# Performance work log

Hardware: AMD Instinct MI355X
Metric: run time of the kernel (lower is better)

The kernel has to match this reference:

```python
import jax, jax.numpy as jnp
import numpy as np

N = 50000
E = 800000
IN_DIM = 128
HIDDEN = 256
HEADS = 8
HEAD_DIM = HIDDEN // HEADS  # 32
NUM_CLASSES = 40
NEG_SLOPE = 0.2


def setup_inputs() -> dict:
    key = jax.random.key(0)
    ks = jax.random.split(key, 16)
    x = jax.random.normal(ks[0], (N, IN_DIM), dtype=jnp.float32)
    edge_index = jax.random.randint(ks[1], (2, E), 0, N, dtype=jnp.int64)

    def glorot(k, shape, fan_in):
        return jax.random.normal(k, shape, dtype=jnp.float32) / np.sqrt(fan_in)

    # layer 1: in -> heads*head_dim (concat)
    W1 = glorot(ks[2], (IN_DIM, HEADS * HEAD_DIM), IN_DIM)
    as1 = glorot(ks[3], (HEADS, HEAD_DIM), HEAD_DIM)
    ad1 = glorot(ks[4], (HEADS, HEAD_DIM), HEAD_DIM)
    b1 = jnp.zeros((HEADS * HEAD_DIM,), dtype=jnp.float32)
    # layer 2: hidden -> heads*head_dim (concat)
    W2 = glorot(ks[5], (HIDDEN, HEADS * HEAD_DIM), HIDDEN)
    as2 = glorot(ks[6], (HEADS, HEAD_DIM), HEAD_DIM)
    ad2 = glorot(ks[7], (HEADS, HEAD_DIM), HEAD_DIM)
    b2 = jnp.zeros((HEADS * HEAD_DIM,), dtype=jnp.float32)
    # layer 3: hidden -> num_classes, 1 head, no concat (mean == identity for 1 head)
    W3 = glorot(ks[8], (HIDDEN, 1 * NUM_CLASSES), HIDDEN)
    as3 = glorot(ks[9], (1, NUM_CLASSES), NUM_CLASSES)
    ad3 = glorot(ks[10], (1, NUM_CLASSES), NUM_CLASSES)
    b3 = jnp.zeros((NUM_CLASSES,), dtype=jnp.float32)
    return {"x": x, "edge_index": edge_index,
            "W1": W1, "as1": as1, "ad1": ad1, "b1": b1,
            "W2": W2, "as2": as2, "ad2": ad2, "b2": b2,
            "W3": W3, "as3": as3, "ad3": ad3, "b3": b3}


def _segment_softmax(logits, seg, n):
    # logits: [E, H]; softmax per destination node
    m = jax.ops.segment_max(logits, seg, num_segments=n)
    m = jnp.where(jnp.isfinite(m), m, 0.0)  # empty segments -> 0
    e = jnp.exp(logits - m[seg])
    s = jax.ops.segment_sum(e, seg, num_segments=n)
    return e / (s[seg] + 1e-16)


def _gat_layer(x, src, dst, W, a_src, a_dst, b, heads, concat):
    n = x.shape[0]
    h = (x @ W).reshape(n, heads, -1)                    # [N, H, D]
    al_s = jnp.einsum('nhd,hd->nh', h, a_src)            # [N, H]
    al_d = jnp.einsum('nhd,hd->nh', h, a_dst)            # [N, H]
    e = jax.nn.leaky_relu(al_s[src] + al_d[dst], NEG_SLOPE)  # [E, H]
    alpha = _segment_softmax(e, dst, n)                  # [E, H]
    msg = h[src] * alpha[..., None]                      # [E, H, D]
    out = jax.ops.segment_sum(msg, dst, num_segments=n)  # [N, H, D]
    out = out.reshape(n, -1) if concat else out.mean(axis=1)
    return out + b


def reference(x, edge_index, W1, as1, ad1, b1, W2, as2, ad2, b2, W3, as3, ad3, b3):
    # add self loops (PyG GATConv default)
    loops = jnp.arange(N, dtype=edge_index.dtype)
    src = jnp.concatenate([edge_index[0], loops])
    dst = jnp.concatenate([edge_index[1], loops])
    # eval mode: dropout is a no-op
    h = _gat_layer(x, src, dst, W1, as1, ad1, b1, HEADS, True)
    h = jax.nn.elu(h)
    h = _gat_layer(h, src, dst, W2, as2, ad2, b2, HEADS, True)
    h = jax.nn.elu(h)
    out = _gat_layer(h, src, dst, W3, as3, ad3, b3, 1, False)
    return out
```

## Files before the change

### kernel.cpp

```cpp
#include <hip/hip_runtime.h>
#include <hip/hip_bf16.h>

#define NEG_SLOPE 0.2f

typedef __attribute__((ext_vector_type(8))) short bf16x8;
typedef __attribute__((ext_vector_type(4))) float f32x4;

__device__ __forceinline__ unsigned short f2bf(float v) {
    union { float f; unsigned int u; } x; x.f = v;
    unsigned int r = x.u + 0x7fffu + ((x.u >> 16) & 1u);
    return (unsigned short)(r >> 16);
}
__device__ __forceinline__ float bf2f(unsigned short b) {
    union { unsigned int u; float f; } x; x.u = ((unsigned int)b) << 16;
    return x.f;
}


__global__ void count_edges_k(const int* __restrict__ ei, int E, int n, int* __restrict__ cnt) {
    int e = blockIdx.x * 256 + threadIdx.x;
    int ET = E + n;
    if (e >= ET) return;
    int d = (e < E) ? ei[E + e] : (e - E);
    atomicAdd(&cnt[d], 1);
}

__global__ void scan1_k(const int* __restrict__ cnt, int* __restrict__ row_ptr,
                        int* __restrict__ bsums, int n) {
    __shared__ int sd[256];
    int b = blockIdx.x, t = threadIdx.x;
    int base = b * 1024 + t * 4;
    int v[4];
    int loc = 0;
#pragma unroll
    for (int j = 0; j < 4; ++j) {
        v[j] = (base + j < n) ? cnt[base + j] : 0;
        loc += v[j];
    }
    sd[t] = loc;
    __syncthreads();
    for (int off = 1; off < 256; off <<= 1) {
        int x = (t >= off) ? sd[t - off] : 0;
        __syncthreads();
        sd[t] += x;
        __syncthreads();
    }
    int run = sd[t] - loc;
    if (t == 255) bsums[b] = sd[t];
#pragma unroll
    for (int j = 0; j < 4; ++j) {
        if (base + j < n) row_ptr[base + j] = run;
        run += v[j];
    }
}

__global__ void scan2_k(int* __restrict__ bsums, int nb) {
    if (threadIdx.x == 0 && blockIdx.x == 0) {
        int run = 0;
        for (int i = 0; i < nb; ++i) { int x = bsums[i]; bsums[i] = run; run += x; }
    }
}

__global__ void scan3_k(int* __restrict__ row_ptr, int* __restrict__ pos,
                        const int* __restrict__ bsums, int n, int total) {
    int idx = blockIdx.x * 256 + threadIdx.x;
    if (idx < n) {
        int vv = row_ptr[idx] + bsums[idx >> 10];
        row_ptr[idx] = vv;
        pos[idx] = vv;
    } else if (idx == n) {
        row_ptr[n] = total;
    }
}

__global__ void scatter_edges_k(const int* __restrict__ ei, int E, int n,
                                int* __restrict__ pos, int* __restrict__ srcs) {
    int e = blockIdx.x * 256 + threadIdx.x;
    int ET = E + n;
    if (e >= ET) return;
    int s, d;
    if (e < E) { s = ei[e]; d = ei[E + e]; }
    else       { s = e - E; d = e - E; }
    int idx = atomicAdd(&pos[d], 1);
    srcs[idx] = s;
}


#define R1 (128 * 256)
#define R2 (256 * 256)
#define R3 (256 * 128)

__global__ void convert_w_all_k(const float* __restrict__ W1, const float* __restrict__ W2,
                                const float* __restrict__ W3,
                                unsigned short* __restrict__ b1h, unsigned short* __restrict__ b1l,
                                unsigned short* __restrict__ b2h, unsigned short* __restrict__ b2l,
                                unsigned short* __restrict__ b3h, unsigned short* __restrict__ b3l) {
    int idx = blockIdx.x * 256 + threadIdx.x;
    float v;
    unsigned short* dh;
    unsigned short* dl;
    int o;
    if (idx < R1) {
        int k = idx >> 8, c = idx & 255;
        v = W1[idx]; dh = b1h; dl = b1l; o = c * 128 + k;
    } else if (idx < R1 + R2) {
        int j = idx - R1;
        int k = j >> 8, c = j & 255;
        v = W2[j]; dh = b2h; dl = b2l; o = c * 256 + k;
    } else if (idx < R1 + R2 + R3) {
        int j = idx - (R1 + R2);
        int k = j >> 7, c = j & 127;
        v = (c < 40) ? W3[k * 40 + c] : 0.f;
        dh = b3h; dl = b3l; o = c * 256 + k;
    } else {
        return;
    }
    unsigned short h = f2bf(v);
    dh[o] = h;
    dl[o] = f2bf(v - bf2f(h));
}


#define GPAD 40

__global__ __launch_bounds__(256) void mfma_gemm_k(const float* __restrict__ A,
                                                   const unsigned short* __restrict__ Bh,
                                                   const unsigned short* __restrict__ Bl,
                                                   unsigned short* __restrict__ Cb,
                                                   int M, int K, int Nc) {
    __shared__ unsigned short Ash[128][GPAD];
    __shared__ unsigned short Asl[128][GPAD];
    __shared__ unsigned short Bsh[128][GPAD];
    __shared__ unsigned short Bsl[128][GPAD];

    int bm = blockIdx.y * 128;
    int bn = blockIdx.x * 128;
    int t = threadIdx.x;
    int w = t >> 6, l = t & 63;
    int wm = w >> 1, wn = w & 1;
    int lr = l & 15, lk = (l >> 4) * 8;

    int srow = t >> 1;
    int skh  = (t & 1) * 16;

    f32x4 acc[4][4];
#pragma unroll
    for (int i = 0; i < 4; ++i)
#pragma unroll
        for (int j = 0; j < 4; ++j)
            acc[i][j] = (f32x4){0.f, 0.f, 0.f, 0.f};

    const int arow = bm + srow;
    const bool arow_ok = (arow < M);
    const size_t acol_base = (size_t)arow * K + skh;
    const size_t bcol_base = (size_t)(bn + srow) * K + skh;

    for (int k0 = 0; k0 < K; k0 += 32) {
        float vv[16];
        if (arow_ok) {
            const float4* ap = reinterpret_cast<const float4*>(A + acol_base + k0);
#pragma unroll
            for (int q = 0; q < 4; ++q) {
                float4 v4 = ap[q];
                vv[4 * q + 0] = v4.x; vv[4 * q + 1] = v4.y;
                vv[4 * q + 2] = v4.z; vv[4 * q + 3] = v4.w;
            }
        } else {
#pragma unroll
            for (int q = 0; q < 16; ++q) vv[q] = 0.f;
        }
        unsigned int hw[8], lw[8];
#pragma unroll
        for (int q = 0; q < 8; ++q) {
            unsigned short h0 = f2bf(vv[2 * q]);
            unsigned short h1 = f2bf(vv[2 * q + 1]);
            unsigned short l0 = f2bf(vv[2 * q] - bf2f(h0));
            unsigned short l1 = f2bf(vv[2 * q + 1] - bf2f(h1));
            hw[q] = (unsigned int)h0 | ((unsigned int)h1 << 16);
            lw[q] = (unsigned int)l0 | ((unsigned int)l1 << 16);
        }
        __syncthreads();
        {
            uint4* dh = reinterpret_cast<uint4*>(&Ash[srow][skh]);
            uint4* dl = reinterpret_cast<uint4*>(&Asl[srow][skh]);
            dh[0] = make_uint4(hw[0], hw[1], hw[2], hw[3]);
            dh[1] = make_uint4(hw[4], hw[5], hw[6], hw[7]);
            dl[0] = make_uint4(lw[0], lw[1], lw[2], lw[3]);
            dl[1] = make_uint4(lw[4], lw[5], lw[6], lw[7]);
        }
        {
            const uint4* sh = reinterpret_cast<const uint4*>(Bh + bcol_base + k0);
            const uint4* sl = reinterpret_cast<const uint4*>(Bl + bcol_base + k0);
            uint4* dh = reinterpret_cast<uint4*>(&Bsh[srow][skh]);
            uint4* dl = reinterpret_cast<uint4*>(&Bsl[srow][skh]);
            dh[0] = sh[0]; dh[1] = sh[1];
            dl[0] = sl[0]; dl[1] = sl[1];
        }
        __syncthreads();

        bf16x8 ah[4], al[4], bh[4], bl[4];
#pragma unroll
        for (int i = 0; i < 4; ++i) {
            int r = wm * 64 + i * 16 + lr;
            ah[i] = *reinterpret_cast<const bf16x8*>(&Ash[r][lk]);
            al[i] = *reinterpret_cast<const bf16x8*>(&Asl[r][lk]);
        }
#pragma unroll
        for (int j = 0; j < 4; ++j) {
            int c = wn * 64 + j * 16 + lr;
            bh[j] = *reinterpret_cast<const bf16x8*>(&Bsh[c][lk]);
            bl[j] = *reinterpret_cast<const bf16x8*>(&Bsl[c][lk]);
        }
#pragma unroll
        for (int i = 0; i < 4; ++i)
#pragma unroll
            for (int j = 0; j < 4; ++j) {
                acc[i][j] = __builtin_amdgcn_mfma_f32_16x16x32_bf16(ah[i], bh[j], acc[i][j], 0, 0, 0);
                acc[i][j] = __builtin_amdgcn_mfma_f32_16x16x32_bf16(ah[i], bl[j], acc[i][j], 0, 0, 0);
                acc[i][j] = __builtin_amdgcn_mfma_f32_16x16x32_bf16(al[i], bh[j], acc[i][j], 0, 0, 0);
            }
    }

#pragma unroll
    for (int i = 0; i < 4; ++i) {
#pragma unroll
        for (int r = 0; r < 4; ++r) {
            int row_g = bm + wm * 64 + i * 16 + (l >> 4) * 4 + r;
            if (row_g >= M) continue;
#pragma unroll
            for (int j = 0; j < 4; ++j) {
                int col_g = bn + wn * 64 + j * 16 + lr;
                Cb[(size_t)row_g * Nc + col_g] = f2bf(acc[i][j][r]);
            }
        }
    }
}


__global__ __launch_bounds__(256) void gemm_bf16a_k(const unsigned short* __restrict__ A,
                                                    const unsigned short* __restrict__ Bh,
                                                    const unsigned short* __restrict__ Bl,
                                                    unsigned short* __restrict__ Cb,
                                                    int M, int K, int Nc) {
    __shared__ unsigned short As[128][GPAD];
    __shared__ unsigned short Bsh[128][GPAD];
    __shared__ unsigned short Bsl[128][GPAD];

    int bm = blockIdx.y * 128;
    int bn = blockIdx.x * 128;
    int t = threadIdx.x;
    int w = t >> 6, l = t & 63;
    int wm = w >> 1, wn = w & 1;
    int lr = l & 15, lk = (l >> 4) * 8;

    int srow = t >> 1;
    int skh  = (t & 1) * 16;

    f32x4 acc[4][4];
#pragma unroll
    for (int i = 0; i < 4; ++i)
#pragma unroll
        for (int j = 0; j < 4; ++j)
            acc[i][j] = (f32x4){0.f, 0.f, 0.f, 0.f};

    const int arow = bm + srow;
    const bool arow_ok = (arow < M);
    const size_t acol_base = (size_t)arow * K + skh;
    const size_t bcol_base = (size_t)(bn + srow) * K + skh;

    for (int k0 = 0; k0 < K; k0 += 32) {
        __syncthreads();
        {
            uint4* da = reinterpret_cast<uint4*>(&As[srow][skh]);
            if (arow_ok) {
                const uint4* sa = reinterpret_cast<const uint4*>(A + acol_base + k0);
                da[0] = sa[0]; da[1] = sa[1];
            } else {
                da[0] = make_uint4(0u, 0u, 0u, 0u);
                da[1] = make_uint4(0u, 0u, 0u, 0u);
            }
            const uint4* sh = reinterpret_cast<const uint4*>(Bh + bcol_base + k0);
            const uint4* sl = reinterpret_cast<const uint4*>(Bl + bcol_base + k0);
            uint4* dh = reinterpret_cast<uint4*>(&Bsh[srow][skh]);
            uint4* dl = reinterpret_cast<uint4*>(&Bsl[srow][skh]);
            dh[0] = sh[0]; dh[1] = sh[1];
            dl[0] = sl[0]; dl[1] = sl[1];
        }
        __syncthreads();

        bf16x8 ah[4], bh[4], bl[4];
#pragma unroll
        for (int i = 0; i < 4; ++i) {
            int r = wm * 64 + i * 16 + lr;
            ah[i] = *reinterpret_cast<const bf16x8*>(&As[r][lk]);
        }
#pragma unroll
        for (int j = 0; j < 4; ++j) {
            int c = wn * 64 + j * 16 + lr;
            bh[j] = *reinterpret_cast<const bf16x8*>(&Bsh[c][lk]);
            bl[j] = *reinterpret_cast<const bf16x8*>(&Bsl[c][lk]);
        }
#pragma unroll
        for (int i = 0; i < 4; ++i)
#pragma unroll
            for (int j = 0; j < 4; ++j) {
                acc[i][j] = __builtin_amdgcn_mfma_f32_16x16x32_bf16(ah[i], bh[j], acc[i][j], 0, 0, 0);
                acc[i][j] = __builtin_amdgcn_mfma_f32_16x16x32_bf16(ah[i], bl[j], acc[i][j], 0, 0, 0);
            }
    }

#pragma unroll
    for (int i = 0; i < 4; ++i) {
#pragma unroll
        for (int r = 0; r < 4; ++r) {
            int row_g = bm + wm * 64 + i * 16 + (l >> 4) * 4 + r;
            if (row_g >= M) continue;
#pragma unroll
            for (int j = 0; j < 4; ++j) {
                int col_g = bn + wn * 64 + j * 16 + lr;
                Cb[(size_t)row_g * Nc + col_g] = f2bf(acc[i][j][r]);
            }
        }
    }
}


__global__ __launch_bounds__(256) void compute_al_k(const unsigned short* __restrict__ h,
                                                    const float* __restrict__ a_src,
                                                    const float* __restrict__ a_dst,
                                                    float* __restrict__ al_s,
                                                    float* __restrict__ al_d, int n) {
    int gw = blockIdx.x * 4 + (threadIdx.x >> 6);
    int nw = gridDim.x * 4;
    int lane = threadIdx.x & 63;
    float4 asv = reinterpret_cast<const float4*>(a_src)[lane];
    float4 adv = reinterpret_cast<const float4*>(a_dst)[lane];
    for (int node = gw; node < n; node += nw) {
        ushort4 v = reinterpret_cast<const ushort4*>(h + (size_t)node * 256)[lane];
        float ps = bf2f(v.x) * asv.x + bf2f(v.y) * asv.y + bf2f(v.z) * asv.z + bf2f(v.w) * asv.w;
        float pd = bf2f(v.x) * adv.x + bf2f(v.y) * adv.y + bf2f(v.z) * adv.z + bf2f(v.w) * adv.w;
#pragma unroll
        for (int off = 1; off < 8; off <<= 1) {
            ps += __shfl_xor(ps, off, 64);
            pd += __shfl_xor(pd, off, 64);
        }
        if ((lane & 7) == 0) {
            al_s[node * 8 + (lane >> 3)] = ps;
            al_d[node * 8 + (lane >> 3)] = pd;
        }
    }
}

__global__ void compute_al3_k(const unsigned short* __restrict__ h,
                              const float* __restrict__ a_src, const float* __restrict__ a_dst,
                              float* __restrict__ al_s, float* __restrict__ al_d, int n) {
    int wid = threadIdx.x >> 6, lane = threadIdx.x & 63;
    int node = blockIdx.x * 4 + wid;
    if (node >= n) return;
    float hv = (lane < 40) ? bf2f(h[(size_t)node * 128 + lane]) : 0.f;
    float ps = (lane < 40) ? hv * a_src[lane] : 0.f;
    float pd = (lane < 40) ? hv * a_dst[lane] : 0.f;
#pragma unroll
    for (int off = 32; off; off >>= 1) {
        ps += __shfl_xor(ps, off, 64);
        pd += __shfl_xor(pd, off, 64);
    }
    if (lane == 0) { al_s[node] = ps; al_d[node] = pd; }
}


__global__ __launch_bounds__(256) void edge_softmax_k(const float* __restrict__ al_s,
                                                      const float* __restrict__ al_d,
                                                      const int* __restrict__ row_ptr,
                                                      const int* __restrict__ srcs,
                                                      float* __restrict__ w,
                                                      float* __restrict__ inv, int n8) {
    int tid = blockIdx.x * 256 + threadIdx.x;
    if (tid >= n8) return;
    int dst = tid >> 3, hd = tid & 7;
    int beg = row_ptr[dst], end = row_ptr[dst + 1];
    float ald = al_d[tid];

    float m = -1e30f;
    int i = beg;
    for (; i + 2 <= end; i += 2) {
        int s0 = srcs[i], s1 = srcs[i + 1];
        float l0 = al_s[s0 * 8 + hd] + ald;
        float l1 = al_s[s1 * 8 + hd] + ald;
        l0 = (l0 > 0.f) ? l0 : NEG_SLOPE * l0;
        l1 = (l1 > 0.f) ? l1 : NEG_SLOPE * l1;
        m = fmaxf(m, fmaxf(l0, l1));
    }
    if (i < end) {
        int s0 = srcs[i];
        float l0 = al_s[s0 * 8 + hd] + ald;
        l0 = (l0 > 0.f) ? l0 : NEG_SLOPE * l0;
        m = fmaxf(m, l0);
    }

    float sw = 0.f;
    i = beg;
    for (; i + 2 <= end; i += 2) {
        int s0 = srcs[i], s1 = srcs[i + 1];
        float l0 = al_s[s0 * 8 + hd] + ald;
        float l1 = al_s[s1 * 8 + hd] + ald;
        l0 = (l0 > 0.f) ? l0 : NEG_SLOPE * l0;
        l1 = (l1 > 0.f) ? l1 : NEG_SLOPE * l1;
        float e0 = __expf(l0 - m);
        float e1 = __expf(l1 - m);
        w[(size_t)i * 8 + hd] = e0;
        w[(size_t)(i + 1) * 8 + hd] = e1;
        sw += e0 + e1;
    }
    if (i < end) {
        int s = srcs[i];
        float l = al_s[s * 8 + hd] + ald;
        l = (l > 0.f) ? l : NEG_SLOPE * l;
        float e = __expf(l - m);
        w[(size_t)i * 8 + hd] = e;
        sw += e;
    }
    inv[tid] = 1.f / (sw + 1e-16f);
}

__global__ __launch_bounds__(256) void edge_softmax3_k(const float* __restrict__ al_s,
                                                       const float* __restrict__ al_d,
                                                       const int* __restrict__ row_ptr,
                                                       const int* __restrict__ srcs,
                                                       float* __restrict__ w,
                                                       float* __restrict__ inv, int n) {
    int dst = blockIdx.x * 256 + threadIdx.x;
    if (dst >= n) return;
    int beg = row_ptr[dst], end = row_ptr[dst + 1];
    float ald = al_d[dst];

    float m = -1e30f;
    int i = beg;
    for (; i + 2 <= end; i += 2) {
        int s0 = srcs[i], s1 = srcs[i + 1];
        float l0 = al_s[s0] + ald;
        float l1 = al_s[s1] + ald;
        l0 = (l0 > 0.f) ? l0 : NEG_SLOPE * l0;
        l1 = (l1 > 0.f) ? l1 : NEG_SLOPE * l1;
        m = fmaxf(m, fmaxf(l0, l1));
    }
    if (i < end) {
        int s0 = srcs[i];
        float l0 = al_s[s0] + ald;
        l0 = (l0 > 0.f) ? l0 : NEG_SLOPE * l0;
        m = fmaxf(m, l0);
    }

    float sw = 0.f;
    for (i = beg; i < end; ++i) {
        int s = srcs[i];
        float l = al_s[s] + ald;
        l = (l > 0.f) ? l : NEG_SLOPE * l;
        float e = __expf(l - m);
        w[i] = e;
        sw += e;
    }
    inv[dst] = 1.f / (sw + 1e-16f);
}


template <bool ELU>
__global__ __launch_bounds__(256) void gat_gather_k(const unsigned short* __restrict__ h,
                                                    const float* __restrict__ w,
                                                    const float* __restrict__ inv,
                                                    const int* __restrict__ row_ptr,
                                                    const int* __restrict__ srcs,
                                                    const float* __restrict__ bias,
                                                    unsigned short* __restrict__ out, int n) {
    int gw = blockIdx.x * 4 + (threadIdx.x >> 6);
    int nw = gridDim.x * 4;
    int lane = threadIdx.x & 63;
    int hd = lane >> 3;
    const ushort4* hp = reinterpret_cast<const ushort4*>(h);
    float4 b4 = reinterpret_cast<const float4*>(bias)[lane];

    for (int dst = gw; dst < n; dst += nw) {
        int beg = row_ptr[dst], end = row_ptr[dst + 1];
        float4 acc = make_float4(0.f, 0.f, 0.f, 0.f);
        int i = beg;
        for (; i + 4 <= end; i += 4) {
            int s0 = srcs[i + 0], s1 = srcs[i + 1], s2 = srcs[i + 2], s3 = srcs[i + 3];
            float w0 = w[(size_t)(i + 0) * 8 + hd];
            float w1 = w[(size_t)(i + 1) * 8 + hd];
            float w2 = w[(size_t)(i + 2) * 8 + hd];
            float w3 = w[(size_t)(i + 3) * 8 + hd];
            ushort4 v0 = hp[(size_t)s0 * 64 + lane];
            ushort4 v1 = hp[(size_t)s1 * 64 + lane];
            ushort4 v2 = hp[(size_t)s2 * 64 + lane];
            ushort4 v3 = hp[(size_t)s3 * 64 + lane];
            acc.x = fmaf(w0, bf2f(v0.x), acc.x);
            acc.y = fmaf(w0, bf2f(v0.y), acc.y);
            acc.z = fmaf(w0, bf2f(v0.z), acc.z);
            acc.w = fmaf(w0, bf2f(v0.w), acc.w);
            acc.x = fmaf(w1, bf2f(v1.x), acc.x);
            acc.y = fmaf(w1, bf2f(v1.y), acc.y);
            acc.z = fmaf(w1, bf2f(v1.z), acc.z);
            acc.w = fmaf(w1, bf2f(v1.w), acc.w);
            acc.x = fmaf(w2, bf2f(v2.x), acc.x);
            acc.y = fmaf(w2, bf2f(v2.y), acc.y);
            acc.z = fmaf(w2, bf2f(v2.z), acc.z);
            acc.w = fmaf(w2, bf2f(v2.w), acc.w);
            acc.x = fmaf(w3, bf2f(v3.x), acc.x);
            acc.y = fmaf(w3, bf2f(v3.y), acc.y);
            acc.z = fmaf(w3, bf2f(v3.z), acc.z);
            acc.w = fmaf(w3, bf2f(v3.w), acc.w);
        }
        for (; i < end; ++i) {
            int s = srcs[i];
            float wgt = w[(size_t)i * 8 + hd];
            ushort4 v = hp[(size_t)s * 64 + lane];
            acc.x = fmaf(wgt, bf2f(v.x), acc.x);
            acc.y = fmaf(wgt, bf2f(v.y), acc.y);
            acc.z = fmaf(wgt, bf2f(v.z), acc.z);
            acc.w = fmaf(wgt, bf2f(v.w), acc.w);
        }

        float iv = inv[dst * 8 + hd];
        float4 o;
        o.x = acc.x * iv + b4.x;
        o.y = acc.y * iv + b4.y;
        o.z = acc.z * iv + b4.z;
        o.w = acc.w * iv + b4.w;
        if (ELU) {
            o.x = (o.x > 0.f) ? o.x : expm1f(o.x);
            o.y = (o.y > 0.f) ? o.y : expm1f(o.y);
            o.z = (o.z > 0.f) ? o.z : expm1f(o.z);
            o.w = (o.w > 0.f) ? o.w : expm1f(o.w);
        }
        ushort4 ob;
        ob.x = f2bf(o.x); ob.y = f2bf(o.y); ob.z = f2bf(o.z); ob.w = f2bf(o.w);
        reinterpret_cast<ushort4*>(out + (size_t)dst * 256)[lane] = ob;
    }
}

__global__ __launch_bounds__(256) void gat_gather3_k(const unsigned short* __restrict__ h,
                                                     const float* __restrict__ w,
                                                     const float* __restrict__ inv,
                                                     const int* __restrict__ row_ptr,
                                                     const int* __restrict__ srcs,
                                                     const float* __restrict__ bias,
                                                     float* __restrict__ out, int n) {
    int gw = blockIdx.x * 4 + (threadIdx.x >> 6);
    int nw = gridDim.x * 4;
    int lane = threadIdx.x & 63;
    int es = lane >> 4, cl = lane & 15;

    for (int dst = gw; dst < n; dst += nw) {
        int beg = row_ptr[dst], end = row_ptr[dst + 1];
        float4 acc = make_float4(0.f, 0.f, 0.f, 0.f);
        for (int i = beg; i < end; i += 4) {
            int idx = i + es;
            bool ok = (idx < end);
            int s = ok ? srcs[idx] : srcs[beg];
            float wgt = ok ? w[idx] : 0.f;
            ushort4 v = reinterpret_cast<const ushort4*>(h + (size_t)s * 128)[cl];
            acc.x = fmaf(wgt, bf2f(v.x), acc.x);
            acc.y = fmaf(wgt, bf2f(v.y), acc.y);
            acc.z = fmaf(wgt, bf2f(v.z), acc.z);
            acc.w = fmaf(wgt, bf2f(v.w), acc.w);
        }
#pragma unroll
        for (int off = 16; off <= 32; off <<= 1) {
            acc.x += __shfl_xor(acc.x, off, 64);
            acc.y += __shfl_xor(acc.y, off, 64);
            acc.z += __shfl_xor(acc.z, off, 64);
            acc.w += __shfl_xor(acc.w, off, 64);
        }
        if (es == 0 && cl < 10) {
            float iv = inv[dst];
            int c = cl * 4;
            float4 b4 = *reinterpret_cast<const float4*>(bias + c);
            float4 o;
            o.x = acc.x * iv + b4.x;
            o.y = acc.y * iv + b4.y;
            o.z = acc.z * iv + b4.z;
            o.w = acc.w * iv + b4.w;
            *reinterpret_cast<float4*>(out + (size_t)dst * 40 + c) = o;
        }
    }
}


extern "C" void kernel_launch(void* const* d_in, const int* in_sizes, int n_in,
                              void* d_out, int out_size, void* d_ws, size_t ws_size,
                              hipStream_t stream) {
    const float* x   = (const float*)d_in[0];
    const int*   ei  = (const int*)d_in[1];
    const float* W1  = (const float*)d_in[2];
    const float* as1 = (const float*)d_in[3];
    const float* ad1 = (const float*)d_in[4];
    const float* b1  = (const float*)d_in[5];
    const float* W2  = (const float*)d_in[6];
    const float* as2 = (const float*)d_in[7];
    const float* ad2 = (const float*)d_in[8];
    const float* b2  = (const float*)d_in[9];
    const float* W3  = (const float*)d_in[10];
    const float* as3 = (const float*)d_in[11];
    const float* ad3 = (const float*)d_in[12];
    const float* b3  = (const float*)d_in[13];

    const int N = in_sizes[0] / 128;
    const int E = in_sizes[1] / 2;
    const int ET = E + N;

    char* ws = (char*)d_ws;
    size_t off = 0;
    auto alloc = [&](size_t bytes) -> void* {
        void* p = ws + off;
        off += (bytes + 255) & ~(size_t)255;
        return p;
    };
    int*   row_ptr = (int*)alloc(sizeof(int) * (N + 1));
    int*   pos     = (int*)alloc(sizeof(int) * N);
    int*   srcs    = (int*)alloc(sizeof(int) * ET);
    int*   bsums   = (int*)alloc(sizeof(int) * 64);
    float* als     = (float*)alloc(sizeof(float) * N * 8);
    float* ald     = (float*)alloc(sizeof(float) * N * 8);
    float* wbuf    = (float*)alloc(sizeof(float) * (size_t)ET * 8);
    float* invb    = (float*)alloc(sizeof(float) * N * 8);
    unsigned short* hb16 = (unsigned short*)alloc(sizeof(unsigned short) * (size_t)N * 256);
    unsigned short* ab16 = (unsigned short*)alloc(sizeof(unsigned short) * (size_t)N * 256);
    unsigned short* wb1h = (unsigned short*)alloc(sizeof(unsigned short) * 128 * 256);
    unsigned short* wb1l = (unsigned short*)alloc(sizeof(unsigned short) * 128 * 256);
    unsigned short* wb2h = (unsigned short*)alloc(sizeof(unsigned short) * 256 * 256);
    unsigned short* wb2l = (unsigned short*)alloc(sizeof(unsigned short) * 256 * 256);
    unsigned short* wb3h = (unsigned short*)alloc(sizeof(unsigned short) * 128 * 256);
    unsigned short* wb3l = (unsigned short*)alloc(sizeof(unsigned short) * 128 * 256);
    (void)ws_size;

    const int nb = (N + 1023) / 1024;
    const int PG = 2048;

    convert_w_all_k<<<(R1 + R2 + R3 + 255) / 256, 256, 0, stream>>>(
        W1, W2, W3, wb1h, wb1l, wb2h, wb2l, wb3h, wb3l);

    hipMemsetAsync(pos, 0, sizeof(int) * N, stream);
    count_edges_k<<<(ET + 255) / 256, 256, 0, stream>>>(ei, E, N, pos);
    scan1_k<<<nb, 256, 0, stream>>>(pos, row_ptr, bsums, N);
    scan2_k<<<1, 64, 0, stream>>>(bsums, nb);
    scan3_k<<<(N + 1 + 255) / 256, 256, 0, stream>>>(row_ptr, pos, bsums, N, ET);
    scatter_edges_k<<<(ET + 255) / 256, 256, 0, stream>>>(ei, E, N, pos, srcs);

    const int gy = (N + 127) / 128;
    const int gagg = (N + 3) / 4;
    const int gsm = (N * 8 + 255) / 256;

    mfma_gemm_k<<<dim3(2, gy), 256, 0, stream>>>(x, wb1h, wb1l, hb16, N, 128, 256);
    compute_al_k<<<PG, 256, 0, stream>>>(hb16, as1, ad1, als, ald, N);
    edge_softmax_k<<<gsm, 256, 0, stream>>>(als, ald, row_ptr, srcs, wbuf, invb, N * 8);
    gat_gather_k<true><<<PG, 256, 0, stream>>>(hb16, wbuf, invb, row_ptr, srcs, b1, ab16, N);

    gemm_bf16a_k<<<dim3(2, gy), 256, 0, stream>>>(ab16, wb2h, wb2l, hb16, N, 256, 256);
    compute_al_k<<<PG, 256, 0, stream>>>(hb16, as2, ad2, als, ald, N);
    edge_softmax_k<<<gsm, 256, 0, stream>>>(als, ald, row_ptr, srcs, wbuf, invb, N * 8);
    gat_gather_k<true><<<PG, 256, 0, stream>>>(hb16, wbuf, invb, row_ptr, srcs, b2, ab16, N);

    gemm_bf16a_k<<<dim3(1, gy), 256, 0, stream>>>(ab16, wb3h, wb3l, hb16, N, 256, 128);
    compute_al3_k<<<gagg, 256, 0, stream>>>(hb16, as3, ad3, als, ald, N);
    edge_softmax3_k<<<(N + 255) / 256, 256, 0, stream>>>(als, ald, row_ptr, srcs, wbuf, invb, N);
    gat_gather3_k<<<PG, 256, 0, stream>>>(hb16, wbuf, invb, row_ptr, srcs, b3, (float*)d_out, N);
}
```

Measured before the change: 427.6 us.

## Parallelize edge softmax per wave and process destination pairs in gather

Edge softmax moves from one thread per (node, head) to one wavefront per node, with lanes strided over edges and shuffle reductions for max and sum. This is meant to fix load imbalance and uncoalesced serial loops over high-degree nodes. The layer-1/2 gather now handles two destination nodes per wave with interleaved predicated 4-edge batches, raising memory-level parallelism. The pair kernel assumes N is even and wastes loads when the two degrees differ; empty segments would read endA-1 out of range, but self-loops rule that out.

Measured after the change: 440.9 us. 1.03x slower.

```diff
diff --git a/kernel.cpp b/kernel.cpp
--- a/kernel.cpp
+++ b/kernel.cpp
@@ -369,109 +369,90 @@
 }
 
 
-__global__ __launch_bounds__(256) void edge_softmax_k(const float* __restrict__ al_s,
-                                                      const float* __restrict__ al_d,
-                                                      const int* __restrict__ row_ptr,
-                                                      const int* __restrict__ srcs,
-                                                      float* __restrict__ w,
-                                                      float* __restrict__ inv, int n8) {
-    int tid = blockIdx.x * 256 + threadIdx.x;
-    if (tid >= n8) return;
-    int dst = tid >> 3, hd = tid & 7;
-    int beg = row_ptr[dst], end = row_ptr[dst + 1];
-    float ald = al_d[tid];
-
-    float m = -1e30f;
-    int i = beg;
-    for (; i + 2 <= end; i += 2) {
-        int s0 = srcs[i], s1 = srcs[i + 1];
-        float l0 = al_s[s0 * 8 + hd] + ald;
-        float l1 = al_s[s1 * 8 + hd] + ald;
-        l0 = (l0 > 0.f) ? l0 : NEG_SLOPE * l0;
-        l1 = (l1 > 0.f) ? l1 : NEG_SLOPE * l1;
-        m = fmaxf(m, fmaxf(l0, l1));
-    }
-    if (i < end) {
-        int s0 = srcs[i];
-        float l0 = al_s[s0 * 8 + hd] + ald;
-        l0 = (l0 > 0.f) ? l0 : NEG_SLOPE * l0;
-        m = fmaxf(m, l0);
-    }
-
-    float sw = 0.f;
-    i = beg;
-    for (; i + 2 <= end; i += 2) {
-        int s0 = srcs[i], s1 = srcs[i + 1];
-        float l0 = al_s[s0 * 8 + hd] + ald;
-        float l1 = al_s[s1 * 8 + hd] + ald;
-        l0 = (l0 > 0.f) ? l0 : NEG_SLOPE * l0;
-        l1 = (l1 > 0.f) ? l1 : NEG_SLOPE * l1;
-        float e0 = __expf(l0 - m);
-        float e1 = __expf(l1 - m);
-        w[(size_t)i * 8 + hd] = e0;
-        w[(size_t)(i + 1) * 8 + hd] = e1;
-        sw += e0 + e1;
-    }
-    if (i < end) {
-        int s = srcs[i];
-        float l = al_s[s * 8 + hd] + ald;
-        l = (l > 0.f) ? l : NEG_SLOPE * l;
-        float e = __expf(l - m);
-        w[(size_t)i * 8 + hd] = e;
-        sw += e;
-    }
-    inv[tid] = 1.f / (sw + 1e-16f);
-}
-
-__global__ __launch_bounds__(256) void edge_softmax3_k(const float* __restrict__ al_s,
-                                                       const float* __restrict__ al_d,
-                                                       const int* __restrict__ row_ptr,
-                                                       const int* __restrict__ srcs,
-                                                       float* __restrict__ w,
-                                                       float* __restrict__ inv, int n) {
-    int dst = blockIdx.x * 256 + threadIdx.x;
-    if (dst >= n) return;
-    int beg = row_ptr[dst], end = row_ptr[dst + 1];
-    float ald = al_d[dst];
-
-    float m = -1e30f;
-    int i = beg;
-    for (; i + 2 <= end; i += 2) {
-        int s0 = srcs[i], s1 = srcs[i + 1];
-        float l0 = al_s[s0] + ald;
-        float l1 = al_s[s1] + ald;
-        l0 = (l0 > 0.f) ? l0 : NEG_SLOPE * l0;
-        l1 = (l1 > 0.f) ? l1 : NEG_SLOPE * l1;
-        m = fmaxf(m, fmaxf(l0, l1));
-    }
-    if (i < end) {
-        int s0 = srcs[i];
-        float l0 = al_s[s0] + ald;
-        l0 = (l0 > 0.f) ? l0 : NEG_SLOPE * l0;
-        m = fmaxf(m, l0);
-    }
-
-    float sw = 0.f;
-    for (i = beg; i < end; ++i) {
-        int s = srcs[i];
-        float l = al_s[s] + ald;
-        l = (l > 0.f) ? l : NEG_SLOPE * l;
-        float e = __expf(l - m);
-        w[i] = e;
-        sw += e;
-    }
-    inv[dst] = 1.f / (sw + 1e-16f);
+__global__ __launch_bounds__(256) void edge_softmax_wave_k(const float* __restrict__ al_s,
+                                                           const float* __restrict__ al_d,
+                                                           const int* __restrict__ row_ptr,
+                                                           const int* __restrict__ srcs,
+                                                           float* __restrict__ w,
+                                                           float* __restrict__ inv, int n) {
+    int gw = blockIdx.x * 4 + (threadIdx.x >> 6);
+    int nw = gridDim.x * 4;
+    int lane = threadIdx.x & 63;
+    int es = lane >> 3, hd = lane & 7;
+    for (int dst = gw; dst < n; dst += nw) {
+        int beg = row_ptr[dst], end = row_ptr[dst + 1];
+        float ald = al_d[dst * 8 + hd];
+        float m = -1e30f;
+        for (int i = beg + es; i < end; i += 8) {
+            int s = srcs[i];
+            float l = al_s[s * 8 + hd] + ald;
+            l = (l > 0.f) ? l : NEG_SLOPE * l;
+            m = fmaxf(m, l);
+        }
+        m = fmaxf(m, __shfl_xor(m, 8, 64));
+        m = fmaxf(m, __shfl_xor(m, 16, 64));
+        m = fmaxf(m, __shfl_xor(m, 32, 64));
+        float sw = 0.f;
+        for (int i = beg + es; i < end; i += 8) {
+            int s = srcs[i];
+            float l = al_s[s * 8 + hd] + ald;
+            l = (l > 0.f) ? l : NEG_SLOPE * l;
+            float e = __expf(l - m);
+            w[(size_t)i * 8 + hd] = e;
+            sw += e;
+        }
+        sw += __shfl_xor(sw, 8, 64);
+        sw += __shfl_xor(sw, 16, 64);
+        sw += __shfl_xor(sw, 32, 64);
+        if (es == 0) inv[dst * 8 + hd] = 1.f / (sw + 1e-16f);
+    }
+}
+
+__global__ __launch_bounds__(256) void edge_softmax3_wave_k(const float* __restrict__ al_s,
+                                                            const float* __restrict__ al_d,
+                                                            const int* __restrict__ row_ptr,
+                                                            const int* __restrict__ srcs,
+                                                            float* __restrict__ w,
+                                                            float* __restrict__ inv, int n) {
+    int gw = blockIdx.x * 4 + (threadIdx.x >> 6);
+    int nw = gridDim.x * 4;
+    int lane = threadIdx.x & 63;
+    for (int dst = gw; dst < n; dst += nw) {
+        int beg = row_ptr[dst], end = row_ptr[dst + 1];
+        float ald = al_d[dst];
+        float m = -1e30f;
+        for (int i = beg + lane; i < end; i += 64) {
+            int s = srcs[i];
+            float l = al_s[s] + ald;
+            l = (l > 0.f) ? l : NEG_SLOPE * l;
+            m = fmaxf(m, l);
+        }
+#pragma unroll
+        for (int off = 32; off; off >>= 1) m = fmaxf(m, __shfl_xor(m, off, 64));
+        float sw = 0.f;
+        for (int i = beg + lane; i < end; i += 64) {
+            int s = srcs[i];
+            float l = al_s[s] + ald;
+            l = (l > 0.f) ? l : NEG_SLOPE * l;
+            float e = __expf(l - m);
+            w[i] = e;
+            sw += e;
+        }
+#pragma unroll
+        for (int off = 32; off; off >>= 1) sw += __shfl_xor(sw, off, 64);
+        if (lane == 0) inv[dst] = 1.f / (sw + 1e-16f);
+    }
 }
 
 
 template <bool ELU>
-__global__ __launch_bounds__(256) void gat_gather_k(const unsigned short* __restrict__ h,
-                                                    const float* __restrict__ w,
-                                                    const float* __restrict__ inv,
-                                                    const int* __restrict__ row_ptr,
-                                                    const int* __restrict__ srcs,
-                                                    const float* __restrict__ bias,
-                                                    unsigned short* __restrict__ out, int n) {
+__global__ __launch_bounds__(256) void gat_gather_pair_k(const unsigned short* __restrict__ h,
+                                                         const float* __restrict__ w,
+                                                         const float* __restrict__ inv,
+                                                         const int* __restrict__ row_ptr,
+                                                         const int* __restrict__ srcs,
+                                                         const float* __restrict__ bias,
+                                                         unsigned short* __restrict__ out, int npairs) {
     int gw = blockIdx.x * 4 + (threadIdx.x >> 6);
     int nw = gridDim.x * 4;
     int lane = threadIdx.x & 63;
@@ -479,62 +460,73 @@
     const ushort4* hp = reinterpret_cast<const ushort4*>(h);
     float4 b4 = reinterpret_cast<const float4*>(bias)[lane];
 
-    for (int dst = gw; dst < n; dst += nw) {
-        int beg = row_ptr[dst], end = row_ptr[dst + 1];
-        float4 acc = make_float4(0.f, 0.f, 0.f, 0.f);
-        int i = beg;
-        for (; i + 4 <= end; i += 4) {
-            int s0 = srcs[i + 0], s1 = srcs[i + 1], s2 = srcs[i + 2], s3 = srcs[i + 3];
-            float w0 = w[(size_t)(i + 0) * 8 + hd];
-            float w1 = w[(size_t)(i + 1) * 8 + hd];
-            float w2 = w[(size_t)(i + 2) * 8 + hd];
-            float w3 = w[(size_t)(i + 3) * 8 + hd];
-            ushort4 v0 = hp[(size_t)s0 * 64 + lane];
-            ushort4 v1 = hp[(size_t)s1 * 64 + lane];
-            ushort4 v2 = hp[(size_t)s2 * 64 + lane];
-            ushort4 v3 = hp[(size_t)s3 * 64 + lane];
-            acc.x = fmaf(w0, bf2f(v0.x), acc.x);
-            acc.y = fmaf(w0, bf2f(v0.y), acc.y);
-            acc.z = fmaf(w0, bf2f(v0.z), acc.z);
-            acc.w = fmaf(w0, bf2f(v0.w), acc.w);
-            acc.x = fmaf(w1, bf2f(v1.x), acc.x);
-            acc.y = fmaf(w1, bf2f(v1.y), acc.y);
-            acc.z = fmaf(w1, bf2f(v1.z), acc.z);
-            acc.w = fmaf(w1, bf2f(v1.w), acc.w);
-            acc.x = fmaf(w2, bf2f(v2.x), acc.x);
-            acc.y = fmaf(w2, bf2f(v2.y), acc.y);
-            acc.z = fmaf(w2, bf2f(v2.z), acc.z);
-            acc.w = fmaf(w2, bf2f(v2.w), acc.w);
-            acc.x = fmaf(w3, bf2f(v3.x), acc.x);
-            acc.y = fmaf(w3, bf2f(v3.y), acc.y);
-            acc.z = fmaf(w3, bf2f(v3.z), acc.z);
-            acc.w = fmaf(w3, bf2f(v3.w), acc.w);
-        }
-        for (; i < end; ++i) {
-            int s = srcs[i];
-            float wgt = w[(size_t)i * 8 + hd];
-            ushort4 v = hp[(size_t)s * 64 + lane];
-            acc.x = fmaf(wgt, bf2f(v.x), acc.x);
-            acc.y = fmaf(wgt, bf2f(v.y), acc.y);
-            acc.z = fmaf(wgt, bf2f(v.z), acc.z);
-            acc.w = fmaf(wgt, bf2f(v.w), acc.w);
-        }
-
-        float iv = inv[dst * 8 + hd];
-        float4 o;
-        o.x = acc.x * iv + b4.x;
-        o.y = acc.y * iv + b4.y;
-        o.z = acc.z * iv + b4.z;
-        o.w = acc.w * iv + b4.w;
+    for (int p = gw; p < npairs; p += nw) {
+        int dstA = 2 * p, dstB = 2 * p + 1;
+        int begA = row_ptr[dstA], endA = row_ptr[dstA + 1], endB = row_ptr[dstB + 1];
+        int begB = endA;
+        float4 accA = make_float4(0.f, 0.f, 0.f, 0.f);
+        float4 accB = make_float4(0.f, 0.f, 0.f, 0.f);
+        int iA = begA, iB = begB;
+        int nbA = (endA - begA + 3) >> 2;
+        int nbB = (endB - begB + 3) >> 2;
+        int nb = (nbA > nbB) ? nbA : nbB;
+        for (int b = 0; b < nb; ++b) {
+            int sA[4], sB[4];
+            float wA[4], wB[4];
+#pragma unroll
+            for (int k = 0; k < 4; ++k) {
+                int ia = iA + k;
+                int idxA = (ia < endA) ? ia : (endA - 1);
+                sA[k] = srcs[idxA];
+                float wa = w[(size_t)idxA * 8 + hd];
+                wA[k] = (ia < endA) ? wa : 0.f;
+                int ib = iB + k;
+                int idxB = (ib < endB) ? ib : (endB - 1);
+                sB[k] = srcs[idxB];
+                float wb = w[(size_t)idxB * 8 + hd];
+                wB[k] = (ib < endB) ? wb : 0.f;
+            }
+            ushort4 vA[4], vB[4];
+#pragma unroll
+            for (int k = 0; k < 4; ++k) vA[k] = hp[(size_t)sA[k] * 64 + lane];
+#pragma unroll
+            for (int k = 0; k < 4; ++k) vB[k] = hp[(size_t)sB[k] * 64 + lane];
+#pragma unroll
+            for (int k = 0; k < 4; ++k) {
+                accA.x = fmaf(wA[k], bf2f(vA[k].x), accA.x);
+                accA.y = fmaf(wA[k], bf2f(vA[k].y), accA.y);
+                accA.z = fmaf(wA[k], bf2f(vA[k].z), accA.z);
+                accA.w = fmaf(wA[k], bf2f(vA[k].w), accA.w);
+                accB.x = fmaf(wB[k], bf2f(vB[k].x), accB.x);
+                accB.y = fmaf(wB[k], bf2f(vB[k].y), accB.y);
+                accB.z = fmaf(wB[k], bf2f(vB[k].z), accB.z);
+                accB.w = fmaf(wB[k], bf2f(vB[k].w), accB.w);
+            }
+            iA += 4; iB += 4;
+        }
+
+        float ivA = inv[dstA * 8 + hd];
+        float ivB = inv[dstB * 8 + hd];
+        float4 oA, oB;
+        oA.x = accA.x * ivA + b4.x; oA.y = accA.y * ivA + b4.y;
+        oA.z = accA.z * ivA + b4.z; oA.w = accA.w * ivA + b4.w;
+        oB.x = accB.x * ivB + b4.x; oB.y = accB.y * ivB + b4.y;
+        oB.z = accB.z * ivB + b4.z; oB.w = accB.w * ivB + b4.w;
         if (ELU) {
-            o.x = (o.x > 0.f) ? o.x : expm1f(o.x);
-            o.y = (o.y > 0.f) ? o.y : expm1f(o.y);
-            o.z = (o.z > 0.f) ? o.z : expm1f(o.z);
-            o.w = (o.w > 0.f) ? o.w : expm1f(o.w);
-        }
-        ushort4 ob;
-        ob.x = f2bf(o.x); ob.y = f2bf(o.y); ob.z = f2bf(o.z); ob.w = f2bf(o.w);
-        reinterpret_cast<ushort4*>(out + (size_t)dst * 256)[lane] = ob;
+            oA.x = (oA.x > 0.f) ? oA.x : expm1f(oA.x);
+            oA.y = (oA.y > 0.f) ? oA.y : expm1f(oA.y);
+            oA.z = (oA.z > 0.f) ? oA.z : expm1f(oA.z);
+            oA.w = (oA.w > 0.f) ? oA.w : expm1f(oA.w);
+            oB.x = (oB.x > 0.f) ? oB.x : expm1f(oB.x);
+            oB.y = (oB.y > 0.f) ? oB.y : expm1f(oB.y);
+            oB.z = (oB.z > 0.f) ? oB.z : expm1f(oB.z);
+            oB.w = (oB.w > 0.f) ? oB.w : expm1f(oB.w);
+        }
+        ushort4 obA, obB;
+        obA.x = f2bf(oA.x); obA.y = f2bf(oA.y); obA.z = f2bf(oA.z); obA.w = f2bf(oA.w);
+        obB.x = f2bf(oB.x); obB.y = f2bf(oB.y); obB.z = f2bf(oB.z); obB.w = f2bf(oB.w);
+        reinterpret_cast<ushort4*>(out + (size_t)dstA * 256)[lane] = obA;
+        reinterpret_cast<ushort4*>(out + (size_t)dstB * 256)[lane] = obB;
     }
 }
 
@@ -648,20 +640,20 @@
 
     const int gy = (N + 127) / 128;
     const int gagg = (N + 3) / 4;
-    const int gsm = (N * 8 + 255) / 256;
+    const int npairs = N / 2;
 
     mfma_gemm_k<<<dim3(2, gy), 256, 0, stream>>>(x, wb1h, wb1l, hb16, N, 128, 256);
     compute_al_k<<<PG, 256, 0, stream>>>(hb16, as1, ad1, als, ald, N);
-    edge_softmax_k<<<gsm, 256, 0, stream>>>(als, ald, row_ptr, srcs, wbuf, invb, N * 8);
-    gat_gather_k<true><<<PG, 256, 0, stream>>>(hb16, wbuf, invb, row_ptr, srcs, b1, ab16, N);
+    edge_softmax_wave_k<<<PG, 256, 0, stream>>>(als, ald, row_ptr, srcs, wbuf, invb, N);
+    gat_gather_pair_k<true><<<PG, 256, 0, stream>>>(hb16, wbuf, invb, row_ptr, srcs, b1, ab16, npairs);
 
     gemm_bf16a_k<<<dim3(2, gy), 256, 0, stream>>>(ab16, wb2h, wb2l, hb16, N, 256, 256);
     compute_al_k<<<PG, 256, 0, stream>>>(hb16, as2, ad2, als, ald, N);
-    edge_softmax_k<<<gsm, 256, 0, stream>>>(als, ald, row_ptr, srcs, wbuf, invb, N * 8);
-    gat_gather_k<true><<<PG, 256, 0, stream>>>(hb16, wbuf, invb, row_ptr, srcs, b2, ab16, N);
+    edge_softmax_wave_k<<<PG, 256, 0, stream>>>(als, ald, row_ptr, srcs, wbuf, invb, N);
+    gat_gather_pair_k<true><<<PG, 256, 0, stream>>>(hb16, wbuf, invb, row_ptr, srcs, b2, ab16, npairs);
 
     gemm_bf16a_k<<<dim3(1, gy), 256, 0, stream>>>(ab16, wb3h, wb3l, hb16, N, 256, 128);
     compute_al3_k<<<gagg, 256, 0, stream>>>(hb16, as3, ad3, als, ald, N);
-    edge_softmax3_k<<<(N + 255) / 256, 256, 0, stream>>>(als, ald, row_ptr, srcs, wbuf, invb, N);
+    edge_softmax3_wave_k<<<PG, 256, 0, stream>>>(als, ald, row_ptr, srcs, wbuf, invb, N);
     gat_gather3_k<<<PG, 256, 0, stream>>>(hb16, wbuf, invb, row_ptr, srcs, b3, (float*)d_out, N);
 }
```

## Store edge weights head-major and gather per head slice in separate blocks

Applied to the files above, without the earlier changes.

The edge softmax now writes attention weights in a head-major [8][ET] layout instead of edge-major [ET][8]. The gather kernel is restructured so each block handles one 32-column head slice. Within a wavefront, four edge slots of 16 lanes each load 4-byte bf16 pairs, and the partial sums are reduced with shuffles. The intent is to keep each block's working set of h columns smaller and more cache-friendly and to give more edge-level parallelism per node. The cost is that srcs and row_ptr are read eight times, the 64-byte per-row accesses are narrower, and only a quarter of the lanes do the final store.

New measurement: 738.8 us. +72.8%, slower.

```diff
diff --git a/kernel.cpp b/kernel.cpp
--- a/kernel.cpp
+++ b/kernel.cpp
@@ -369,17 +369,18 @@
 }
 
 
-__global__ __launch_bounds__(256) void edge_softmax_k(const float* __restrict__ al_s,
-                                                      const float* __restrict__ al_d,
-                                                      const int* __restrict__ row_ptr,
-                                                      const int* __restrict__ srcs,
-                                                      float* __restrict__ w,
-                                                      float* __restrict__ inv, int n8) {
+__global__ __launch_bounds__(256) void edge_softmax_t_k(const float* __restrict__ al_s,
+                                                        const float* __restrict__ al_d,
+                                                        const int* __restrict__ row_ptr,
+                                                        const int* __restrict__ srcs,
+                                                        float* __restrict__ wt,
+                                                        float* __restrict__ inv, int n8, int ET) {
     int tid = blockIdx.x * 256 + threadIdx.x;
     if (tid >= n8) return;
     int dst = tid >> 3, hd = tid & 7;
     int beg = row_ptr[dst], end = row_ptr[dst + 1];
     float ald = al_d[tid];
+    float* wp = wt + (size_t)hd * ET;
 
     float m = -1e30f;
     int i = beg;
@@ -408,8 +409,8 @@
         l1 = (l1 > 0.f) ? l1 : NEG_SLOPE * l1;
         float e0 = __expf(l0 - m);
         float e1 = __expf(l1 - m);
-        w[(size_t)i * 8 + hd] = e0;
-        w[(size_t)(i + 1) * 8 + hd] = e1;
+        wp[i] = e0;
+        wp[i + 1] = e1;
         sw += e0 + e1;
     }
     if (i < end) {
@@ -417,7 +418,7 @@
         float l = al_s[s * 8 + hd] + ald;
         l = (l > 0.f) ? l : NEG_SLOPE * l;
         float e = __expf(l - m);
-        w[(size_t)i * 8 + hd] = e;
+        wp[i] = e;
         sw += e;
     }
     inv[tid] = 1.f / (sw + 1e-16f);
@@ -465,76 +466,49 @@
 
 
 template <bool ELU>
-__global__ __launch_bounds__(256) void gat_gather_k(const unsigned short* __restrict__ h,
-                                                    const float* __restrict__ w,
-                                                    const float* __restrict__ inv,
-                                                    const int* __restrict__ row_ptr,
-                                                    const int* __restrict__ srcs,
-                                                    const float* __restrict__ bias,
-                                                    unsigned short* __restrict__ out, int n) {
-    int gw = blockIdx.x * 4 + (threadIdx.x >> 6);
-    int nw = gridDim.x * 4;
-    int lane = threadIdx.x & 63;
-    int hd = lane >> 3;
-    const ushort4* hp = reinterpret_cast<const ushort4*>(h);
-    float4 b4 = reinterpret_cast<const float4*>(bias)[lane];
+__global__ __launch_bounds__(256) void gat_gather_slice_k(const unsigned short* __restrict__ h,
+                                                          const float* __restrict__ wt,
+                                                          const float* __restrict__ inv,
+                                                          const int* __restrict__ row_ptr,
+                                                          const int* __restrict__ srcs,
+                                                          const float* __restrict__ bias,
+                                                          unsigned short* __restrict__ out,
+                                                          int n, int ET) {
+    int s = blockIdx.x & 7;
+    int bs = blockIdx.x >> 3;
+    int wid = threadIdx.x >> 6, lane = threadIdx.x & 63;
+    int slot = lane >> 4, cl = lane & 15;
+    int gw = bs * 4 + wid;
+    int nw = (gridDim.x >> 3) * 4;
+    const float* wp = wt + (size_t)s * ET;
+    int colb = s * 32 + cl * 2;
+    float bx = bias[colb], by = bias[colb + 1];
 
     for (int dst = gw; dst < n; dst += nw) {
         int beg = row_ptr[dst], end = row_ptr[dst + 1];
-        float4 acc = make_float4(0.f, 0.f, 0.f, 0.f);
-        int i = beg;
-        for (; i + 4 <= end; i += 4) {
-            int s0 = srcs[i + 0], s1 = srcs[i + 1], s2 = srcs[i + 2], s3 = srcs[i + 3];
-            float w0 = w[(size_t)(i + 0) * 8 + hd];
-            float w1 = w[(size_t)(i + 1) * 8 + hd];
-            float w2 = w[(size_t)(i + 2) * 8 + hd];
-            float w3 = w[(size_t)(i + 3) * 8 + hd];
-            ushort4 v0 = hp[(size_t)s0 * 64 + lane];
-            ushort4 v1 = hp[(size_t)s1 * 64 + lane];
-            ushort4 v2 = hp[(size_t)s2 * 64 + lane];
-            ushort4 v3 = hp[(size_t)s3 * 64 + lane];
-            acc.x = fmaf(w0, bf2f(v0.x), acc.x);
-            acc.y = fmaf(w0, bf2f(v0.y), acc.y);
-            acc.z = fmaf(w0, bf2f(v0.z), acc.z);
-            acc.w = fmaf(w0, bf2f(v0.w), acc.w);
-            acc.x = fmaf(w1, bf2f(v1.x), acc.x);
-            acc.y = fmaf(w1, bf2f(v1.y), acc.y);
-            acc.z = fmaf(w1, bf2f(v1.z), acc.z);
-            acc.w = fmaf(w1, bf2f(v1.w), acc.w);
-            acc.x = fmaf(w2, bf2f(v2.x), acc.x);
-            acc.y = fmaf(w2, bf2f(v2.y), acc.y);
-            acc.z = fmaf(w2, bf2f(v2.z), acc.z);
-            acc.w = fmaf(w2, bf2f(v2.w), acc.w);
-            acc.x = fmaf(w3, bf2f(v3.x), acc.x);
-            acc.y = fmaf(w3, bf2f(v3.y), acc.y);
-            acc.z = fmaf(w3, bf2f(v3.z), acc.z);
-            acc.w = fmaf(w3, bf2f(v3.w), acc.w);
-        }
-        for (; i < end; ++i) {
-            int s = srcs[i];
-            float wgt = w[(size_t)i * 8 + hd];
-            ushort4 v = hp[(size_t)s * 64 + lane];
-            acc.x = fmaf(wgt, bf2f(v.x), acc.x);
-            acc.y = fmaf(wgt, bf2f(v.y), acc.y);
-            acc.z = fmaf(wgt, bf2f(v.z), acc.z);
-            acc.w = fmaf(wgt, bf2f(v.w), acc.w);
-        }
-
-        float iv = inv[dst * 8 + hd];
-        float4 o;
-        o.x = acc.x * iv + b4.x;
-        o.y = acc.y * iv + b4.y;
-        o.z = acc.z * iv + b4.z;
-        o.w = acc.w * iv + b4.w;
-        if (ELU) {
-            o.x = (o.x > 0.f) ? o.x : expm1f(o.x);
-            o.y = (o.y > 0.f) ? o.y : expm1f(o.y);
-            o.z = (o.z > 0.f) ? o.z : expm1f(o.z);
-            o.w = (o.w > 0.f) ? o.w : expm1f(o.w);
-        }
-        ushort4 ob;
-        ob.x = f2bf(o.x); ob.y = f2bf(o.y); ob.z = f2bf(o.z); ob.w = f2bf(o.w);
-        reinterpret_cast<ushort4*>(out + (size_t)dst * 256)[lane] = ob;
+        float ax = 0.f, ay = 0.f;
+        for (int i = beg + slot; i < end; i += 4) {
+            int se = srcs[i];
+            float wgt = wp[i];
+            unsigned int v = *reinterpret_cast<const unsigned int*>(h + (size_t)se * 256 + colb);
+            ax = fmaf(wgt, bf2f((unsigned short)(v & 0xffffu)), ax);
+            ay = fmaf(wgt, bf2f((unsigned short)(v >> 16)), ay);
+        }
+        ax += __shfl_xor(ax, 16, 64);
+        ay += __shfl_xor(ay, 16, 64);
+        ax += __shfl_xor(ax, 32, 64);
+        ay += __shfl_xor(ay, 32, 64);
+        if (slot == 0) {
+            float iv = inv[dst * 8 + s];
+            float ox = ax * iv + bx;
+            float oy = ay * iv + by;
+            if (ELU) {
+                ox = (ox > 0.f) ? ox : expm1f(ox);
+                oy = (oy > 0.f) ? oy : expm1f(oy);
+            }
+            unsigned int o = (unsigned int)f2bf(ox) | ((unsigned int)f2bf(oy) << 16);
+            *reinterpret_cast<unsigned int*>(out + (size_t)dst * 256 + colb) = o;
+        }
     }
 }
 
@@ -652,13 +626,13 @@
 
     mfma_gemm_k<<<dim3(2, gy), 256, 0, stream>>>(x, wb1h, wb1l, hb16, N, 128, 256);
     compute_al_k<<<PG, 256, 0, stream>>>(hb16, as1, ad1, als, ald, N);
-    edge_softmax_k<<<gsm, 256, 0, stream>>>(als, ald, row_ptr, srcs, wbuf, invb, N * 8);
-    gat_gather_k<true><<<PG, 256, 0, stream>>>(hb16, wbuf, invb, row_ptr, srcs, b1, ab16, N);
+    edge_softmax_t_k<<<gsm, 256, 0, stream>>>(als, ald, row_ptr, srcs, wbuf, invb, N * 8, ET);
+    gat_gather_slice_k<true><<<PG, 256, 0, stream>>>(hb16, wbuf, invb, row_ptr, srcs, b1, ab16, N, ET);
 
     gemm_bf16a_k<<<dim3(2, gy), 256, 0, stream>>>(ab16, wb2h, wb2l, hb16, N, 256, 256);
     compute_al_k<<<PG, 256, 0, stream>>>(hb16, as2, ad2, als, ald, N);
-    edge_softmax_k<<<gsm, 256, 0, stream>>>(als, ald, row_ptr, srcs, wbuf, invb, N * 8);
-    gat_gather_k<true><<<PG, 256, 0, stream>>>(hb16, wbuf, invb, row_ptr, srcs, b2, ab16, N);
+    edge_softmax_t_k<<<gsm, 256, 0, stream>>>(als, ald, row_ptr, srcs, wbuf, invb, N * 8, ET);
+    gat_gather_slice_k<true><<<PG, 256, 0, stream>>>(hb16, wbuf, invb, row_ptr, srcs, b2, ab16, N, ET);
 
     gemm_bf16a_k<<<dim3(1, gy), 256, 0, stream>>>(ab16, wb3h, wb3l, hb16, N, 256, 128);
     compute_al3_k<<<gagg, 256, 0, stream>>>(hb16, as3, ad3, als, ald, N);
```
